# Optimization experiments

Measured on AMD Instinct MI355X. Metric: run time of the kernel, lower is better.

Reference implementation:

```python
import jax, jax.numpy as jnp
import numpy as np

NUM_HEADS = 12
WINDOW = (14, 14)


def gen_relative_position_index(ws):
    num_rel = (2 * ws[0] - 1) * (2 * ws[1] - 1) + 3
    coords = np.stack(np.meshgrid(np.arange(ws[0]), np.arange(ws[1]), indexing='ij'))
    cf = coords.reshape(2, -1)  # [2, Wh*Ww]
    rel = cf[:, :, None] - cf[:, None, :]  # [2, A, A]
    rel = rel.transpose(1, 2, 0).astype(np.int64)  # [A, A, 2]
    rel[..., 0] += ws[0] - 1
    rel[..., 1] += ws[1] - 1
    rel[..., 0] *= 2 * ws[1] - 1
    area = ws[0] * ws[1]
    idx = np.zeros((area + 1, area + 1), dtype=np.int64)
    idx[1:, 1:] = rel.sum(-1)
    idx[0, :] = num_rel - 3
    idx[:, 0] = num_rel - 2
    idx[0, 0] = num_rel - 1
    return idx


def setup_inputs() -> dict:
    key = jax.random.key(0)
    ks = jax.random.split(key, 7)
    B, N, C = 128, WINDOW[0] * WINDOW[1] + 1, 768
    num_rel = (2 * WINDOW[0] - 1) * (2 * WINDOW[1] - 1) + 3  # 732
    s = 0.02
    return {
        'x': jax.random.normal(ks[0], (B, N, C), jnp.float32),
        'qkv_w': jax.random.normal(ks[1], (3 * C, C), jnp.float32) * s,
        'q_bias': jax.random.normal(ks[2], (C,), jnp.float32) * s,
        'v_bias': jax.random.normal(ks[3], (C,), jnp.float32) * s,
        'rel_pos_table': jax.random.normal(ks[4], (num_rel, NUM_HEADS), jnp.float32) * s,
        'proj_w': jax.random.normal(ks[5], (C, C), jnp.float32) * s,
        'proj_b': jax.random.normal(ks[6], (C,), jnp.float32) * s,
        'rel_index': jnp.asarray(gen_relative_position_index(WINDOW)),
    }


def reference(x, qkv_w, q_bias, v_bias, rel_pos_table, proj_w, proj_b, rel_index):
    B, N, C = x.shape
    H = NUM_HEADS
    hd = C // H
    scale = hd ** -0.5
    # qkv projection with (q_bias, zeros, v_bias) composite bias
    bias = jnp.concatenate([q_bias, jnp.zeros_like(q_bias), v_bias])
    qkv = x @ qkv_w.T + bias  # [B, N, 3C]
    qkv = qkv.reshape(B, N, 3, H, hd).transpose(2, 0, 3, 1, 4)  # [3, B, H, N, hd]
    q, k, v = qkv[0], qkv[1], qkv[2]
    # gather relative position bias: [N, N, H] -> [H, N, N]
    rel_bias = rel_pos_table[rel_index.reshape(-1)].reshape(N, N, H).transpose(2, 0, 1)
    attn = jnp.einsum('bhnd,bhmd->bhnm', q * scale, k) + rel_bias[None]
    attn = jax.nn.softmax(attn, axis=-1)
    out = jnp.einsum('bhnm,bhmd->bhnd', attn, v)  # [B, H, N, hd]
    out = out.transpose(0, 2, 1, 3).reshape(B, N, C)
    return out @ proj_w.T + proj_b
```

## Files before the change

### kernel.cpp

```cpp
#include <hip/hip_runtime.h>

typedef unsigned short u16;
typedef __attribute__((ext_vector_type(8))) short short8;
typedef __attribute__((ext_vector_type(8))) __bf16 bf16x8;
typedef __attribute__((ext_vector_type(4))) float floatx4;

#define BATCH 128
#define SEQ 197
#define CH 768
#define NH 12
#define HD 64
#define MROWS (BATCH * SEQ)

__device__ __forceinline__ floatx4 mfma16(short8 a, short8 b, floatx4 c) {
  return __builtin_amdgcn_mfma_f32_16x16x32_bf16(
      __builtin_bit_cast(bf16x8, a), __builtin_bit_cast(bf16x8, b), c, 0, 0, 0);
}

__device__ __forceinline__ u16 f2bf(float f) {
  unsigned u = __builtin_bit_cast(unsigned, f);
  return (u16)((u + 0x7fffu + ((u >> 16) & 1u)) >> 16);
}

__device__ __forceinline__ void async16(const u16* g, u16* s) {
  __builtin_amdgcn_global_load_lds((const __attribute__((address_space(1))) void*)g,
                                   (__attribute__((address_space(3))) void*)s, 16, 0, 0);
}

__global__ __launch_bounds__(256) void preproc(const float4* __restrict__ x, ushort4* __restrict__ xo, int n0,
                                               const float4* __restrict__ w1, ushort4* __restrict__ w1o, int n1,
                                               const float4* __restrict__ w2, ushort4* __restrict__ w2o, int n2,
                                               const int* __restrict__ idx, const float* __restrict__ table,
                                               float* __restrict__ relb) {
  int i = blockIdx.x * 256 + threadIdx.x;
  const float4* in; ushort4* out; int j;
  if (i < n0) { in = x; out = xo; j = i; }
  else if (i < n0 + n1) { in = w1; out = w1o; j = i - n0; }
  else if (i < n0 + n1 + n2) { in = w2; out = w2o; j = i - n0 - n1; }
  else {
    int t = i - (n0 + n1 + n2);
    if (t < SEQ * SEQ) {
      int id = idx[t];
      const float* row = table + id * NH;
#pragma unroll
      for (int h = 0; h < NH; h++) relb[h * (SEQ * SEQ) + t] = row[h];
    }
    return;
  }
  float4 v = in[j];
  ushort4 o;
  o.x = f2bf(v.x); o.y = f2bf(v.y); o.z = f2bf(v.z); o.w = f2bf(v.w);
  out[j] = o;
}

__global__ __launch_bounds__(256, 2) void gemm_qkv(const u16* __restrict__ A,
                                                   const u16* __restrict__ W,
                                                   const float* __restrict__ qb,
                                                   const float* __restrict__ vb,
                                                   u16* __restrict__ q_buf,
                                                   u16* __restrict__ k_buf,
                                                   u16* __restrict__ v_buf) {
  __shared__ u16 S[3][(128 + 256) * 32];
  const int BUF = (128 + 256) * 32;
  const int BOFF = 128 * 32;
  const int NT = CH / 32;
  int tid = threadIdx.x;
  int wave = tid >> 6, lane = tid & 63, quad = lane >> 4, c16 = lane & 15;
  int wm = wave >> 1, wn = wave & 1;

  int nwg = gridDim.x;
  int orig = blockIdx.x;
  int xcd = orig & 7, pos = orig >> 3;
  int qq = nwg >> 3, rr = nwg & 7;
  int lid = (xcd < rr ? xcd * (qq + 1) : rr * (qq + 1) + (xcd - rr) * qq) + pos;
  int mblk = lid / 9, nblk = lid - mblk * 9;
  int m0 = mblk * 128, n0 = nblk * 256;

  int lrow = lane >> 2;
  int lcol = (((lane & 3) ^ ((lane >> 3) & 3))) * 8;
  const u16* Ag0 = A + (size_t)(m0 + wave * 32 + lrow) * CH + lcol;
  const u16* Ag1 = Ag0 + (size_t)16 * CH;
  const u16* Bg0 = W + (size_t)(n0 + wave * 64 + lrow) * CH + lcol;
  const u16* Bg1 = Bg0 + (size_t)16 * CH;
  const u16* Bg2 = Bg0 + (size_t)32 * CH;
  const u16* Bg3 = Bg0 + (size_t)48 * CH;
  int aw0 = (wave * 32) * 32;
  int aw1 = (wave * 32 + 16) * 32;
  int bw0 = BOFF + (wave * 64) * 32;
  int bw1 = BOFF + (wave * 64 + 16) * 32;
  int bw2 = BOFF + (wave * 64 + 32) * 32;
  int bw3 = BOFF + (wave * 64 + 48) * 32;
  int fsl = (quad ^ ((c16 >> 1) & 3)) * 8;
  int aro = (wm * 64 + c16) * 32 + fsl;
  int bro = BOFF + (wn * 128 + c16) * 32 + fsl;

  floatx4 acc[4][8] = {};
  u16* sbase = &S[0][0];

#define STAGE(kk_, sn_)                                                        \
  do {                                                                         \
    async16(Ag0 + (kk_), (sn_) + aw0);                                         \
    async16(Ag1 + (kk_), (sn_) + aw1);                                         \
    async16(Bg0 + (kk_), (sn_) + bw0);                                         \
    async16(Bg1 + (kk_), (sn_) + bw1);                                         \
    async16(Bg2 + (kk_), (sn_) + bw2);                                         \
    async16(Bg3 + (kk_), (sn_) + bw3);                                         \
  } while (0)

#define COMPUTE(sc_)                                                           \
  do {                                                                         \
    const u16* sc = (sc_);                                                     \
    short8 af[4], bfr[8];                                                      \
    _Pragma("unroll")                                                          \
    for (int i = 0; i < 4; i++) af[i] = *(const short8*)(sc + aro + i * 16 * 32); \
    _Pragma("unroll")                                                          \
    for (int j = 0; j < 8; j++) bfr[j] = *(const short8*)(sc + bro + j * 16 * 32); \
    _Pragma("unroll")                                                          \
    for (int i = 0; i < 4; i++)                                                \
      _Pragma("unroll")                                                        \
      for (int j = 0; j < 8; j++) acc[i][j] = mfma16(af[i], bfr[j], acc[i][j]); \
  } while (0)

  STAGE(0, sbase);
  STAGE(32, sbase + BUF);
  asm volatile("s_waitcnt vmcnt(6)" ::: "memory");
  __builtin_amdgcn_s_barrier();
  asm volatile("" ::: "memory");

  int cc = 0, ss = 2;
  for (int kt = 0; kt < NT - 2; ++kt) {
    STAGE((kt + 2) * 32, sbase + ss * BUF);
    COMPUTE(sbase + cc * BUF);
    asm volatile("s_waitcnt vmcnt(6)" ::: "memory");
    __builtin_amdgcn_s_barrier();
    asm volatile("" ::: "memory");
    cc = cc == 2 ? 0 : cc + 1;
    ss = ss == 2 ? 0 : ss + 1;
  }
  COMPUTE(sbase + cc * BUF);
  asm volatile("s_waitcnt vmcnt(0)" ::: "memory");
  __builtin_amdgcn_s_barrier();
  asm volatile("" ::: "memory");
  cc = cc == 2 ? 0 : cc + 1;
  COMPUTE(sbase + cc * BUF);

#undef STAGE
#undef COMPUTE

#pragma unroll
  for (int j = 0; j < 8; j++) {
    int gcol = n0 + wn * 128 + j * 16 + c16;
    int t = gcol / CH;
    int rem = gcol - t * CH;
    int h = rem >> 6, d = rem & 63;
    float badd = (t == 0) ? qb[rem] : (t == 2 ? vb[rem] : 0.0f);
    u16* dst = (t == 0) ? q_buf : (t == 1 ? k_buf : v_buf);
#pragma unroll
    for (int i = 0; i < 4; i++) {
#pragma unroll
      for (int r = 0; r < 4; r++) {
        int grow = m0 + wm * 64 + i * 16 + quad * 4 + r;
        int bb = grow / SEQ;
        int n = grow - bb * SEQ;
        dst[(((size_t)bb * NH + h) * SEQ + n) * HD + d] = f2bf(acc[i][j][r] + badd);
      }
    }
  }
}

#define PS 232
#define VS 264

__global__ __launch_bounds__(256, 2) void attn(const u16* __restrict__ q_buf,
                                               const u16* __restrict__ k_buf,
                                               const u16* __restrict__ v_buf,
                                               const float* __restrict__ relb,
                                               u16* __restrict__ attn_out) {
  __shared__ u16 Vt[64 * VS];
  __shared__ u16 P[4 * 16 * PS];

  int h = blockIdx.x, b = blockIdx.y;
  int tid = threadIdx.x, wave = tid >> 6, lane = tid & 63, quad = lane >> 4, c16 = lane & 15;
  size_t bh = (size_t)b * NH + h;
  const u16* Q = q_buf + bh * SEQ * HD;
  const u16* Kp = k_buf + bh * SEQ * HD;
  const u16* Vp = v_buf + bh * SEQ * HD;
  const float* RB = relb + (size_t)h * (SEQ * SEQ);

  {
    int mrow = tid >> 3, dbase = (tid & 7) * 8;
#pragma unroll
    for (int i = 0; i < 7; i++) {
      int m = mrow + 32 * i;
      if (m < SEQ) {
        ushort4 v0 = *(const ushort4*)(Vp + m * HD + dbase);
        ushort4 v1 = *(const ushort4*)(Vp + m * HD + dbase + 4);
        Vt[(dbase + 0) * VS + m] = v0.x;
        Vt[(dbase + 1) * VS + m] = v0.y;
        Vt[(dbase + 2) * VS + m] = v0.z;
        Vt[(dbase + 3) * VS + m] = v0.w;
        Vt[(dbase + 4) * VS + m] = v1.x;
        Vt[(dbase + 5) * VS + m] = v1.y;
        Vt[(dbase + 6) * VS + m] = v1.z;
        Vt[(dbase + 7) * VS + m] = v1.w;
      } else {
#pragma unroll
        for (int dd = 0; dd < 8; dd++) Vt[(dbase + dd) * VS + m] = 0;
      }
    }
  }
  __syncthreads();

  u16* Pw = P + wave * 16 * PS;
  for (int rt = wave; rt < 13; rt += 4) {
    int q0 = rt * 16;
    int qr = min(q0 + c16, SEQ - 1);
    short8 qa0 = *(const short8*)(Q + qr * HD + quad * 8);
    short8 qa1 = *(const short8*)(Q + qr * HD + 32 + quad * 8);

    floatx4 sacc[13];
    __builtin_amdgcn_s_setprio(1);
#pragma unroll
    for (int nt = 0; nt < 13; nt++) {
      int mc = min(nt * 16 + c16, SEQ - 1);
      floatx4 a = {0.f, 0.f, 0.f, 0.f};
      a = mfma16(qa0, *(const short8*)(Kp + mc * HD + quad * 8), a);
      a = mfma16(qa1, *(const short8*)(Kp + mc * HD + 32 + quad * 8), a);
      sacc[nt] = a;
    }
    __builtin_amdgcn_s_setprio(0);

#pragma unroll
    for (int r = 0; r < 4; r++) {
      int rq = min(q0 + quad * 4 + r, SEQ - 1);
      const float* RBr = RB + (size_t)rq * SEQ;
      float mx = -1e30f;
#pragma unroll
      for (int nt = 0; nt < 13; nt++) {
        int m = nt * 16 + c16;
        float s = -1e30f;
        if (m < SEQ) s = sacc[nt][r] * 0.125f + RBr[m];
        sacc[nt][r] = s;
        mx = fmaxf(mx, s);
      }
      mx = fmaxf(mx, __shfl_xor(mx, 1));
      mx = fmaxf(mx, __shfl_xor(mx, 2));
      mx = fmaxf(mx, __shfl_xor(mx, 4));
      mx = fmaxf(mx, __shfl_xor(mx, 8));
      float sum = 0.f;
#pragma unroll
      for (int nt = 0; nt < 13; nt++) {
        float e = __expf(sacc[nt][r] - mx);
        sacc[nt][r] = e;
        sum += e;
      }
      sum += __shfl_xor(sum, 1);
      sum += __shfl_xor(sum, 2);
      sum += __shfl_xor(sum, 4);
      sum += __shfl_xor(sum, 8);
      float inv = 1.f / sum;
      int prow = (quad * 4 + r) * PS;
#pragma unroll
      for (int nt = 0; nt < 13; nt++)
        Pw[prow + nt * 16 + c16] = f2bf(sacc[nt][r] * inv);
      Pw[prow + 208 + c16] = 0;
    }

    floatx4 oacc[4] = {};
    __builtin_amdgcn_s_setprio(1);
#pragma unroll
    for (int ks = 0; ks < 7; ks++) {
      short8 a = *(const short8*)(Pw + c16 * PS + ks * 32 + quad * 8);
#pragma unroll
      for (int dt = 0; dt < 4; dt++) {
        short8 bb = *(const short8*)(Vt + (dt * 16 + c16) * VS + ks * 32 + quad * 8);
        oacc[dt] = mfma16(a, bb, oacc[dt]);
      }
    }
    __builtin_amdgcn_s_setprio(0);
#pragma unroll
    for (int dt = 0; dt < 4; dt++) {
      int d = dt * 16 + c16;
#pragma unroll
      for (int r = 0; r < 4; r++) {
        int grow = q0 + quad * 4 + r;
        if (grow < SEQ)
          attn_out[((size_t)b * SEQ + grow) * CH + h * HD + d] = f2bf(oacc[dt][r]);
      }
    }
  }
}

__global__ __launch_bounds__(256, 2) void gemm_proj(const u16* __restrict__ A,
                                                    const u16* __restrict__ W,
                                                    const float* __restrict__ bias,
                                                    float* __restrict__ out) {
  __shared__ u16 S[3][(128 + 256) * 32];
  const int BUF = (128 + 256) * 32;
  const int BOFF = 128 * 32;
  const int NT = CH / 32;
  int tid = threadIdx.x;
  int wave = tid >> 6, lane = tid & 63, quad = lane >> 4, c16 = lane & 15;
  int wm = wave >> 1, wn = wave & 1;

  int nwg = gridDim.x;
  int orig = blockIdx.x;
  int xcd = orig & 7, pos = orig >> 3;
  int qq = nwg >> 3, rr = nwg & 7;
  int lid = (xcd < rr ? xcd * (qq + 1) : rr * (qq + 1) + (xcd - rr) * qq) + pos;
  int mblk = lid / 3, nblk = lid - mblk * 3;
  int m0 = mblk * 128, n0 = nblk * 256;

  int lrow = lane >> 2;
  int lcol = (((lane & 3) ^ ((lane >> 3) & 3))) * 8;
  const u16* Ag0 = A + (size_t)(m0 + wave * 32 + lrow) * CH + lcol;
  const u16* Ag1 = Ag0 + (size_t)16 * CH;
  const u16* Bg0 = W + (size_t)(n0 + wave * 64 + lrow) * CH + lcol;
  const u16* Bg1 = Bg0 + (size_t)16 * CH;
  const u16* Bg2 = Bg0 + (size_t)32 * CH;
  const u16* Bg3 = Bg0 + (size_t)48 * CH;
  int aw0 = (wave * 32) * 32;
  int aw1 = (wave * 32 + 16) * 32;
  int bw0 = BOFF + (wave * 64) * 32;
  int bw1 = BOFF + (wave * 64 + 16) * 32;
  int bw2 = BOFF + (wave * 64 + 32) * 32;
  int bw3 = BOFF + (wave * 64 + 48) * 32;
  int fsl = (quad ^ ((c16 >> 1) & 3)) * 8;
  int aro = (wm * 64 + c16) * 32 + fsl;
  int bro = BOFF + (wn * 128 + c16) * 32 + fsl;

  floatx4 acc[4][8] = {};
  u16* sbase = &S[0][0];

#define STAGE(kk_, sn_)                                                        \
  do {                                                                         \
    async16(Ag0 + (kk_), (sn_) + aw0);                                         \
    async16(Ag1 + (kk_), (sn_) + aw1);                                         \
    async16(Bg0 + (kk_), (sn_) + bw0);                                         \
    async16(Bg1 + (kk_), (sn_) + bw1);                                         \
    async16(Bg2 + (kk_), (sn_) + bw2);                                         \
    async16(Bg3 + (kk_), (sn_) + bw3);                                         \
  } while (0)

#define COMPUTE(sc_)                                                           \
  do {                                                                         \
    const u16* sc = (sc_);                                                     \
    short8 af[4], bfr[8];                                                      \
    _Pragma("unroll")                                                          \
    for (int i = 0; i < 4; i++) af[i] = *(const short8*)(sc + aro + i * 16 * 32); \
    _Pragma("unroll")                                                          \
    for (int j = 0; j < 8; j++) bfr[j] = *(const short8*)(sc + bro + j * 16 * 32); \
    _Pragma("unroll")                                                          \
    for (int i = 0; i < 4; i++)                                                \
      _Pragma("unroll")                                                        \
      for (int j = 0; j < 8; j++) acc[i][j] = mfma16(af[i], bfr[j], acc[i][j]); \
  } while (0)

  STAGE(0, sbase);
  STAGE(32, sbase + BUF);
  asm volatile("s_waitcnt vmcnt(6)" ::: "memory");
  __builtin_amdgcn_s_barrier();
  asm volatile("" ::: "memory");

  int cc = 0, ss = 2;
  for (int kt = 0; kt < NT - 2; ++kt) {
    STAGE((kt + 2) * 32, sbase + ss * BUF);
    COMPUTE(sbase + cc * BUF);
    asm volatile("s_waitcnt vmcnt(6)" ::: "memory");
    __builtin_amdgcn_s_barrier();
    asm volatile("" ::: "memory");
    cc = cc == 2 ? 0 : cc + 1;
    ss = ss == 2 ? 0 : ss + 1;
  }
  COMPUTE(sbase + cc * BUF);
  asm volatile("s_waitcnt vmcnt(0)" ::: "memory");
  __builtin_amdgcn_s_barrier();
  asm volatile("" ::: "memory");
  cc = cc == 2 ? 0 : cc + 1;
  COMPUTE(sbase + cc * BUF);

#undef STAGE
#undef COMPUTE

#pragma unroll
  for (int j = 0; j < 8; j++) {
    int gcol = n0 + wn * 128 + j * 16 + c16;
    float bj = bias[gcol];
#pragma unroll
    for (int i = 0; i < 4; i++)
#pragma unroll
      for (int r = 0; r < 4; r++) {
        int grow = m0 + wm * 64 + i * 16 + quad * 4 + r;
        out[(size_t)grow * CH + gcol] = acc[i][j][r] + bj;
      }
  }
}

extern "C" void kernel_launch(void* const* d_in, const int* in_sizes, int n_in,
                              void* d_out, int out_size, void* d_ws, size_t ws_size,
                              hipStream_t stream) {
  const float* x      = (const float*)d_in[0];
  const float* qkv_w  = (const float*)d_in[1];
  const float* q_bias = (const float*)d_in[2];
  const float* v_bias = (const float*)d_in[3];
  const float* table  = (const float*)d_in[4];
  const float* proj_w = (const float*)d_in[5];
  const float* proj_b = (const float*)d_in[6];
  const int*   rel_ix = (const int*)d_in[7];
  float* out = (float*)d_out;

  char* ws = (char*)d_ws;
  size_t off = 0;
  u16* x_bf  = (u16*)(ws + off); off += (size_t)MROWS * CH * 2;
  u16* wq_bf = (u16*)(ws + off); off += (size_t)3 * CH * CH * 2;
  u16* wp_bf = (u16*)(ws + off); off += (size_t)CH * CH * 2;
  u16* q_buf = (u16*)(ws + off); off += (size_t)MROWS * CH * 2;
  u16* k_buf = (u16*)(ws + off); off += (size_t)MROWS * CH * 2;
  u16* v_buf = (u16*)(ws + off); off += (size_t)MROWS * CH * 2;
  u16* ao_bf = (u16*)(ws + off); off += (size_t)MROWS * CH * 2;
  float* relb = (float*)(ws + off);

  int n0 = MROWS * CH / 4;
  int n1 = 3 * CH * CH / 4;
  int n2 = CH * CH / 4;
  int ntot = n0 + n1 + n2 + SEQ * SEQ;
  preproc<<<(ntot + 255) / 256, 256, 0, stream>>>(
      (const float4*)x, (ushort4*)x_bf, n0,
      (const float4*)qkv_w, (ushort4*)wq_bf, n1,
      (const float4*)proj_w, (ushort4*)wp_bf, n2,
      rel_ix, table, relb);
  gemm_qkv<<<dim3(197 * 9), 256, 0, stream>>>(x_bf, wq_bf, q_bias, v_bias, q_buf, k_buf, v_buf);
  attn<<<dim3(NH, BATCH), 256, 0, stream>>>(q_buf, k_buf, v_buf, relb, ao_bf);
  gemm_proj<<<dim3(197 * 3), 256, 0, stream>>>(ao_bf, wp_bf, proj_b, out);
}
```

Baseline: 385.1 us.

## Store QKV as row-major interleaved buffer and defer softmax normalization to output

```diff
diff --git a/kernel.cpp b/kernel.cpp
--- a/kernel.cpp
+++ b/kernel.cpp
@@ -11,6 +11,7 @@
 #define NH 12
 #define HD 64
 #define MROWS (BATCH * SEQ)
+#define QKVC (3 * CH)
 
 __device__ __forceinline__ floatx4 mfma16(short8 a, short8 b, floatx4 c) {
   return __builtin_amdgcn_mfma_f32_16x16x32_bf16(
@@ -57,9 +58,7 @@
                                                    const u16* __restrict__ W,
                                                    const float* __restrict__ qb,
                                                    const float* __restrict__ vb,
-                                                   u16* __restrict__ q_buf,
-                                                   u16* __restrict__ k_buf,
-                                                   u16* __restrict__ v_buf) {
+                                                   u16* __restrict__ qkv) {
   __shared__ u16 S[3][(128 + 256) * 32];
   const int BUF = (128 + 256) * 32;
   const int BOFF = 128 * 32;
@@ -150,19 +149,13 @@
 #pragma unroll
   for (int j = 0; j < 8; j++) {
     int gcol = n0 + wn * 128 + j * 16 + c16;
-    int t = gcol / CH;
-    int rem = gcol - t * CH;
-    int h = rem >> 6, d = rem & 63;
-    float badd = (t == 0) ? qb[rem] : (t == 2 ? vb[rem] : 0.0f);
-    u16* dst = (t == 0) ? q_buf : (t == 1 ? k_buf : v_buf);
+    float badd = (gcol < CH) ? qb[gcol] : (gcol >= 2 * CH ? vb[gcol - 2 * CH] : 0.0f);
 #pragma unroll
     for (int i = 0; i < 4; i++) {
 #pragma unroll
       for (int r = 0; r < 4; r++) {
         int grow = m0 + wm * 64 + i * 16 + quad * 4 + r;
-        int bb = grow / SEQ;
-        int n = grow - bb * SEQ;
-        dst[(((size_t)bb * NH + h) * SEQ + n) * HD + d] = f2bf(acc[i][j][r] + badd);
+        qkv[(size_t)grow * QKVC + gcol] = f2bf(acc[i][j][r] + badd);
       }
     }
   }
@@ -171,9 +164,7 @@
 #define PS 232
 #define VS 264
 
-__global__ __launch_bounds__(256, 2) void attn(const u16* __restrict__ q_buf,
-                                               const u16* __restrict__ k_buf,
-                                               const u16* __restrict__ v_buf,
+__global__ __launch_bounds__(256, 2) void attn(const u16* __restrict__ qkv,
                                                const float* __restrict__ relb,
                                                u16* __restrict__ attn_out) {
   __shared__ u16 Vt[64 * VS];
@@ -181,10 +172,9 @@
 
   int h = blockIdx.x, b = blockIdx.y;
   int tid = threadIdx.x, wave = tid >> 6, lane = tid & 63, quad = lane >> 4, c16 = lane & 15;
-  size_t bh = (size_t)b * NH + h;
-  const u16* Q = q_buf + bh * SEQ * HD;
-  const u16* Kp = k_buf + bh * SEQ * HD;
-  const u16* Vp = v_buf + bh * SEQ * HD;
+  const u16* Q = qkv + (size_t)b * SEQ * QKVC + h * HD;
+  const u16* Kp = Q + CH;
+  const u16* Vp = Q + 2 * CH;
   const float* RB = relb + (size_t)h * (SEQ * SEQ);
 
   {
@@ -193,8 +183,8 @@
     for (int i = 0; i < 7; i++) {
       int m = mrow + 32 * i;
       if (m < SEQ) {
-        ushort4 v0 = *(const ushort4*)(Vp + m * HD + dbase);
-        ushort4 v1 = *(const ushort4*)(Vp + m * HD + dbase + 4);
+        ushort4 v0 = *(const ushort4*)(Vp + (size_t)m * QKVC + dbase);
+        ushort4 v1 = *(const ushort4*)(Vp + (size_t)m * QKVC + dbase + 4);
         Vt[(dbase + 0) * VS + m] = v0.x;
         Vt[(dbase + 1) * VS + m] = v0.y;
         Vt[(dbase + 2) * VS + m] = v0.z;
@@ -215,8 +205,8 @@
   for (int rt = wave; rt < 13; rt += 4) {
     int q0 = rt * 16;
     int qr = min(q0 + c16, SEQ - 1);
-    short8 qa0 = *(const short8*)(Q + qr * HD + quad * 8);
-    short8 qa1 = *(const short8*)(Q + qr * HD + 32 + quad * 8);
+    short8 qa0 = *(const short8*)(Q + (size_t)qr * QKVC + quad * 8);
+    short8 qa1 = *(const short8*)(Q + (size_t)qr * QKVC + 32 + quad * 8);
 
     floatx4 sacc[13];
     __builtin_amdgcn_s_setprio(1);
@@ -224,12 +214,13 @@
     for (int nt = 0; nt < 13; nt++) {
       int mc = min(nt * 16 + c16, SEQ - 1);
       floatx4 a = {0.f, 0.f, 0.f, 0.f};
-      a = mfma16(qa0, *(const short8*)(Kp + mc * HD + quad * 8), a);
-      a = mfma16(qa1, *(const short8*)(Kp + mc * HD + 32 + quad * 8), a);
+      a = mfma16(qa0, *(const short8*)(Kp + (size_t)mc * QKVC + quad * 8), a);
+      a = mfma16(qa1, *(const short8*)(Kp + (size_t)mc * QKVC + 32 + quad * 8), a);
       sacc[nt] = a;
     }
     __builtin_amdgcn_s_setprio(0);
 
+    float invr[4];
 #pragma unroll
     for (int r = 0; r < 4; r++) {
       int rq = min(q0 + quad * 4 + r, SEQ - 1);
@@ -258,11 +249,11 @@
       sum += __shfl_xor(sum, 2);
       sum += __shfl_xor(sum, 4);
       sum += __shfl_xor(sum, 8);
-      float inv = 1.f / sum;
+      invr[r] = 1.f / sum;
       int prow = (quad * 4 + r) * PS;
 #pragma unroll
       for (int nt = 0; nt < 13; nt++)
-        Pw[prow + nt * 16 + c16] = f2bf(sacc[nt][r] * inv);
+        Pw[prow + nt * 16 + c16] = f2bf(sacc[nt][r]);
       Pw[prow + 208 + c16] = 0;
     }
 
@@ -285,7 +276,7 @@
       for (int r = 0; r < 4; r++) {
         int grow = q0 + quad * 4 + r;
         if (grow < SEQ)
-          attn_out[((size_t)b * SEQ + grow) * CH + h * HD + d] = f2bf(oacc[dt][r]);
+          attn_out[((size_t)b * SEQ + grow) * CH + h * HD + d] = f2bf(oacc[dt][r] * invr[r]);
       }
     }
   }
@@ -411,14 +402,12 @@
 
   char* ws = (char*)d_ws;
   size_t off = 0;
-  u16* x_bf  = (u16*)(ws + off); off += (size_t)MROWS * CH * 2;
-  u16* wq_bf = (u16*)(ws + off); off += (size_t)3 * CH * CH * 2;
-  u16* wp_bf = (u16*)(ws + off); off += (size_t)CH * CH * 2;
-  u16* q_buf = (u16*)(ws + off); off += (size_t)MROWS * CH * 2;
-  u16* k_buf = (u16*)(ws + off); off += (size_t)MROWS * CH * 2;
-  u16* v_buf = (u16*)(ws + off); off += (size_t)MROWS * CH * 2;
-  u16* ao_bf = (u16*)(ws + off); off += (size_t)MROWS * CH * 2;
-  float* relb = (float*)(ws + off);
+  u16* x_bf    = (u16*)(ws + off); off += (size_t)MROWS * CH * 2;
+  u16* wq_bf   = (u16*)(ws + off); off += (size_t)3 * CH * CH * 2;
+  u16* wp_bf   = (u16*)(ws + off); off += (size_t)CH * CH * 2;
+  u16* qkv_buf = (u16*)(ws + off); off += (size_t)MROWS * QKVC * 2;
+  u16* ao_bf   = (u16*)(ws + off); off += (size_t)MROWS * CH * 2;
+  float* relb  = (float*)(ws + off);
 
   int n0 = MROWS * CH / 4;
   int n1 = 3 * CH * CH / 4;
@@ -429,7 +418,7 @@
       (const float4*)qkv_w, (ushort4*)wq_bf, n1,
       (const float4*)proj_w, (ushort4*)wp_bf, n2,
       rel_ix, table, relb);
-  gemm_qkv<<<dim3(197 * 9), 256, 0, stream>>>(x_bf, wq_bf, q_bias, v_bias, q_buf, k_buf, v_buf);
-  attn<<<dim3(NH, BATCH), 256, 0, stream>>>(q_buf, k_buf, v_buf, relb, ao_bf);
+  gemm_qkv<<<dim3(197 * 9), 256, 0, stream>>>(x_bf, wq_bf, q_bias, v_bias, qkv_buf);
+  attn<<<dim3(NH, BATCH), 256, 0, stream>>>(qkv_buf, relb, ao_bf);
   gemm_proj<<<dim3(197 * 3), 256, 0, stream>>>(ao_bf, wp_bf, proj_b, out);
 }
```

Result: faster. 376.3 us (-2.3%).
